# Kernel optimization log

Measured on AMD Instinct MI355X. Metric: run time of the kernel, lower is better.

The kernel has to match this reference:

```python
import jax, jax.numpy as jnp
import numpy as np

B, N, S, K = 16, 16384, 4096, 16
D_PT, D_IN, C_MID, D_OUT = 3, 64, 16, 128
HID = [8, 8]


def _layernorm(x, g, b, eps=1e-5):
    m = x.mean(-1, keepdims=True)
    v = x.var(-1, keepdims=True)
    return (x - m) * jax.lax.rsqrt(v + eps) * g + b


def _gather(feat, idx):
    # feat: [B, C, N], idx: [B, S, K] -> [B, C, S, K]
    return jax.vmap(lambda f, i: f[:, i])(feat, idx)


def setup_inputs() -> dict:
    key = jax.random.key(0)
    ks = jax.random.split(key, 16)
    inp = {
        "xyz": jax.random.normal(ks[0], (B, D_PT, N), jnp.float32),
        "points": jax.random.normal(ks[1], (B, D_IN, N), jnp.float32),
        "new_xyz": jax.random.normal(ks[2], (B, D_PT, S), jnp.float32),
        "nn_idx": jax.random.randint(ks[3], (B, S, K), 0, N, jnp.int32),
    }
    # WeightNet: Linear(3,8)+LN(8), Linear(8,8)+LN(8), Linear(8,16)+LN(16)
    dims = [D_PT] + HID + [C_MID]
    for i in range(3):
        inp[f"w{i}"] = jax.random.normal(ks[4 + i], (dims[i], dims[i + 1]), jnp.float32) * 0.1
        inp[f"b{i}"] = jnp.zeros((dims[i + 1],), jnp.float32)
        inp[f"g{i}"] = jnp.ones((dims[i + 1],), jnp.float32)
        inp[f"be{i}"] = jnp.zeros((dims[i + 1],), jnp.float32)
    last_ch = D_PT + D_IN  # 67
    inp["wl"] = jax.random.normal(ks[8], (C_MID * last_ch, D_OUT), jnp.float32) * 0.02
    inp["bl"] = jnp.zeros((D_OUT,), jnp.float32)
    inp["gl"] = jnp.ones((D_OUT,), jnp.float32)
    inp["bel"] = jnp.zeros((D_OUT,), jnp.float32)
    return inp


def reference(xyz, points, new_xyz, nn_idx,
              w0, b0, g0, be0, w1, b1, g1, be1, w2, b2, g2, be2,
              wl, bl, gl, bel):
    # gather neighbor positions / features: [B, C, S, K]
    grouped_xyz = _gather(xyz, nn_idx)
    gxn = grouped_xyz - new_xyz[:, :, :, None]          # [B, 3, S, K]
    feat = jnp.concatenate([_gather(points, nn_idx), gxn], axis=1)  # [B, 67, S, K]

    # WeightNet on relative coords: MLP over channel dim, layout [B, S, K, 3]
    w = jnp.transpose(gxn, (0, 2, 3, 1))
    for wi, bi, gi, bei in ((w0, b0, g0, be0), (w1, b1, g1, be1), (w2, b2, g2, be2)):
        w = jax.nn.leaky_relu(_layernorm(w @ wi + bi, gi, bei), 0.2)
    # w: [B, S, K, c_mid]

    # weighted aggregation: out[b,s,c,m] = sum_k feat[b,c,s,k] * w[b,s,k,m]
    agg = jnp.einsum("bcsk,bskm->bscm", feat, w).reshape(B, S, -1)  # [B, S, 67*c_mid]

    out = _layernorm(agg @ wl + bl, gl, bel)
    out = jax.nn.leaky_relu(out, 0.2)
    return jnp.transpose(out, (0, 2, 1))  # [B, out_channel, S]
```

## Files before the change

kernel.cpp:

```cpp
#include <hip/hip_runtime.h>

#define B_ 16
#define N_ 16384
#define S_ 4096
#define K_ 16
#define TS 32
#define DOUT 128

typedef __bf16 bf16;
typedef __attribute__((ext_vector_type(8))) __bf16 bf16x8;
typedef __attribute__((ext_vector_type(4))) float f32x4;

__device__ __forceinline__ unsigned pack2(float a, float b) {
  unsigned short ua = __builtin_bit_cast(unsigned short, (bf16)a);
  unsigned short ub = __builtin_bit_cast(unsigned short, (bf16)b);
  return (unsigned)ua | ((unsigned)ub << 16);
}

template <int NCH>
__device__ __forceinline__ void ln_leaky(const float* h, const float* g, const float* e, float* o) {
  float m = 0.f;
#pragma unroll
  for (int j = 0; j < NCH; ++j) m += h[j];
  m *= (1.0f / NCH);
  float v = 0.f;
#pragma unroll
  for (int j = 0; j < NCH; ++j) { float d = h[j] - m; v += d * d; }
  v *= (1.0f / NCH);
  float inv = rsqrtf(v + 1e-5f);
#pragma unroll
  for (int j = 0; j < NCH; ++j) {
    float t = (h[j] - m) * inv * g[j] + e[j];
    o[j] = t < 0.f ? 0.2f * t : t;
  }
}

__global__ void k_fill(float* out, float v) {
  out[blockIdx.x * 256 + threadIdx.x] = v;
}

__global__ __launch_bounds__(256) void k_transpose(const float* __restrict__ pts,
                                                   bf16* __restrict__ pt) {
  int b = blockIdx.y;
  int n0 = blockIdx.x * 256;
  int tc = threadIdx.x & 7;
  int tn = threadIdx.x >> 3;
  const float* src = pts + (size_t)b * 64 * N_ + (size_t)(tc * 8) * N_ + n0 + tn * 8;
  float4 row[8][2];
#pragma unroll
  for (int i = 0; i < 8; ++i) {
    row[i][0] = *(const float4*)(src + (size_t)i * N_);
    row[i][1] = *(const float4*)(src + (size_t)i * N_ + 4);
  }
  bf16* dst = pt + ((size_t)b * N_ + n0 + tn * 8) * 64 + tc * 8;
#pragma unroll
  for (int j = 0; j < 8; ++j) {
    float v[8];
#pragma unroll
    for (int i = 0; i < 8; ++i) {
      float4 q = row[i][j >> 2];
      v[i] = ((j & 3) == 0) ? q.x : ((j & 3) == 1) ? q.y : ((j & 3) == 2) ? q.z : q.w;
    }
    *(uint4*)(dst + (size_t)j * 64) = make_uint4(
        pack2(v[0], v[1]), pack2(v[2], v[3]), pack2(v[4], v[5]), pack2(v[6], v[7]));
  }
}

__global__ void k_wlf(const float* __restrict__ wl, bf16* __restrict__ wlF) {
  int blk = blockIdx.x;
  int kkg = blk % 34;
  int t = blk / 34;
  int tid = threadIdx.x;
  int L = tid >> 2, jp = (tid & 3) * 2;
  int k = kkg * 32 + ((L >> 4) << 3) + jp;
  int n = t * 16 + (L & 15);
  float v0 = (k < 1072) ? wl[(size_t)k * 128 + n] : 0.f;
  float v1 = (k + 1 < 1072) ? wl[(size_t)(k + 1) * 128 + n] : 0.f;
  ((unsigned*)wlF)[(size_t)blk * 256 + tid] = pack2(v0, v1);
}

__global__ __launch_bounds__(256, 4) void k_main(
    const float* __restrict__ xyz, const float* __restrict__ nxyz,
    const int* __restrict__ nnidx,
    const bf16* __restrict__ ptT, const bf16* __restrict__ wlF,
    const float* __restrict__ w0p, const float* __restrict__ b0p,
    const float* __restrict__ g0p, const float* __restrict__ be0p,
    const float* __restrict__ w1p, const float* __restrict__ b1p,
    const float* __restrict__ g1p, const float* __restrict__ be1p,
    const float* __restrict__ w2p, const float* __restrict__ b2p,
    const float* __restrict__ g2p, const float* __restrict__ be2p,
    const float* __restrict__ blp, const float* __restrict__ glp,
    const float* __restrict__ belp, float* __restrict__ out) {
  __shared__ __align__(16) bf16 w_sT[32 * 264];
  __shared__ __align__(16) bf16 feat2[32 * 144];
  __shared__ __align__(16) bf16 aggA[32 * 136];
  __shared__ float nx[3][TS];
  __shared__ float ln_m[TS], ln_i[TS];

  const int tid = threadIdx.x;
  const unsigned Lwg = blockIdx.y * 128u + blockIdx.x;
  const int xcd = (int)(Lwg & 7u);
  const int li = (int)(Lwg >> 3);
  const int b = xcd * 2 + (li >> 7);
  const int s0 = (li & 127) * TS;
  const size_t ibase = ((size_t)b * S_ + s0) * K_;

  if (tid < 96) {
    int c = tid >> 5, j = tid & 31;
    nx[c][j] = nxyz[((size_t)b * 3 + c) * S_ + s0 + j];
  }
  const int ig0 = nnidx[ibase + tid];
  const int ig1 = nnidx[ibase + tid + 256];
  const int iw0 = nnidx[ibase + 2 * tid];
  const int iw1 = nnidx[ibase + 2 * tid + 1];
  __syncthreads();

  float xa[3], xb[3];
  const int ws = tid >> 3;
  const int wk = (tid & 7) * 2;
  {
#pragma unroll
    for (int c = 0; c < 3; ++c) {
      float nv = nx[c][ws];
      xa[c] = xyz[((size_t)b * 3 + c) * N_ + iw0] - nv;
      xb[c] = xyz[((size_t)b * 3 + c) * N_ + iw1] - nv;
    }
    float ya[8], yb[8];
    {
      float h0[8], h1[8];
#pragma unroll
      for (int j = 0; j < 8; ++j) {
        h0[j] = b0p[j] + xa[0] * w0p[j] + xa[1] * w0p[8 + j] + xa[2] * w0p[16 + j];
        h1[j] = b0p[j] + xb[0] * w0p[j] + xb[1] * w0p[8 + j] + xb[2] * w0p[16 + j];
      }
      ln_leaky<8>(h0, g0p, be0p, ya);
      ln_leaky<8>(h1, g0p, be0p, yb);
    }
    {
      float h0[8], h1[8];
#pragma unroll
      for (int j = 0; j < 8; ++j) { h0[j] = b1p[j]; h1[j] = b1p[j]; }
#pragma unroll
      for (int i = 0; i < 8; ++i) {
#pragma unroll
        for (int j = 0; j < 8; ++j) {
          float w = w1p[i * 8 + j];
          h0[j] += ya[i] * w; h1[j] += yb[i] * w;
        }
      }
      ln_leaky<8>(h0, g1p, be1p, ya);
      ln_leaky<8>(h1, g1p, be1p, yb);
    }
    {
      float h0[16], h1[16];
#pragma unroll
      for (int j = 0; j < 16; ++j) { h0[j] = b2p[j]; h1[j] = b2p[j]; }
#pragma unroll
      for (int i = 0; i < 8; ++i) {
#pragma unroll
        for (int j = 0; j < 16; ++j) {
          float w = w2p[i * 16 + j];
          h0[j] += ya[i] * w; h1[j] += yb[i] * w;
        }
      }
      float z0[16], z1[16];
      ln_leaky<16>(h0, g2p, be2p, z0);
      ln_leaky<16>(h1, g2p, be2p, z1);
      bf16* wp = w_sT + ws * 264 + wk;
#pragma unroll
      for (int m = 0; m < 16; ++m)
        *(unsigned*)(wp + m * 16) = pack2(z0[m], z1[m]);
    }
  }

  const int lane = tid & 63;
  const int wv = tid >> 6;
  const int rt = wv & 1;
  const int cw = wv >> 1;
  const int l16 = lane & 15;
  const int q = lane >> 4;
  const bool adiag = ((((lane >> 5) ^ (lane >> 3)) & 1) == 0);
  const int aoff = ((lane >> 3) & 1) * 144 + (lane & 7) * 16 + (q & 1) * 8;
  const int boff = (lane >> 5) * 264 + l16 * 16 + (q & 1) * 8;
  const int soff = (lane >> 5) * 136 + (q & 1) * 64 + l16;
  f32x4 a00 = {0.f, 0.f, 0.f, 0.f};
  f32x4 a01 = a00, a10 = a00, a11 = a00;
  const f32x4 zc = a00;

  const bf16* ptB = ptT + (size_t)b * N_ * 64;
  const int gs0 = tid >> 4, gk = tid & 15;

  uint4 pf0, pf1;
  pf0 = *(const uint4*)(ptB + (size_t)ig0 * 64);
  pf1 = *(const uint4*)(ptB + (size_t)ig1 * 64);

  for (int ch = 0; ch < 9; ++ch) {
    const int nkk = (ch < 8) ? 4 : 2;
    __syncthreads();
    if (ch < 8) {
      bf16 t0[8], t1[8];
      *(uint4*)t0 = pf0;
      *(uint4*)t1 = pf1;
      bf16* f0 = feat2 + gs0 * 144 + gk;
      bf16* f1 = feat2 + (gs0 + 16) * 144 + gk;
#pragma unroll
      for (int c = 0; c < 8; ++c) {
        f0[c * 16] = t0[c];
        f1[c * 16] = t1[c];
      }
    } else {
      bf16* fp = feat2 + ws * 144 + wk;
      *(unsigned*)(fp + 0 * 16) = pack2(xa[0], xb[0]);
      *(unsigned*)(fp + 1 * 16) = pack2(xa[1], xb[1]);
      *(unsigned*)(fp + 2 * 16) = pack2(xa[2], xb[2]);
#pragma unroll
      for (int c = 3; c < 8; ++c) *(unsigned*)(fp + c * 16) = 0u;
    }
    __syncthreads();
    if (ch < 8) {
      int nc = ch + 1;
      if (nc < 8) {
        pf0 = *(const uint4*)(ptB + (size_t)ig0 * 64 + nc * 8);
        pf1 = *(const uint4*)(ptB + (size_t)ig1 * 64 + nc * 8);
      }
    }
#pragma unroll
    for (int pp = 0; pp < 4; ++pp) {
      int s2 = (wv * 4 + pp) * 2;
      uint4 au = *(const uint4*)(feat2 + s2 * 144 + aoff);
      if (!adiag) au = make_uint4(0u, 0u, 0u, 0u);
      bf16x8 af = __builtin_bit_cast(bf16x8, au);
      bf16x8 bw = *(const bf16x8*)(w_sT + s2 * 264 + boff);
      f32x4 d = __builtin_amdgcn_mfma_f32_16x16x32_bf16(af, bw, zc, 0, 0, 0);
      bf16* cp = aggA + s2 * 136 + soff;
#pragma unroll
      for (int r = 0; r < 4; ++r) cp[r * 16] = (bf16)d[r];
    }
    __syncthreads();
    {
      const bf16* arow = aggA + (rt * 16 + l16) * 136 + q * 8;
      const size_t lb = (size_t)lane * 8;
      const size_t kb = (size_t)(ch * 4) * 512;
      const bf16* w0f = wlF + (size_t)(2 * cw + 0) * 17408 + kb + lb;
      const bf16* w1f = wlF + (size_t)(2 * cw + 1) * 17408 + kb + lb;
      const bf16* w2f = wlF + (size_t)(2 * cw + 4) * 17408 + kb + lb;
      const bf16* w3f = wlF + (size_t)(2 * cw + 5) * 17408 + kb + lb;
      for (int kk = 0; kk < nkk; ++kk) {
        bf16x8 af = *(const bf16x8*)(arow + kk * 32);
        bf16x8 bf0 = *(const bf16x8*)(w0f + kk * 512);
        bf16x8 bf1 = *(const bf16x8*)(w1f + kk * 512);
        bf16x8 bf2 = *(const bf16x8*)(w2f + kk * 512);
        bf16x8 bf3 = *(const bf16x8*)(w3f + kk * 512);
        a00 = __builtin_amdgcn_mfma_f32_16x16x32_bf16(af, bf0, a00, 0, 0, 0);
        a01 = __builtin_amdgcn_mfma_f32_16x16x32_bf16(af, bf1, a01, 0, 0, 0);
        a10 = __builtin_amdgcn_mfma_f32_16x16x32_bf16(af, bf2, a10, 0, 0, 0);
        a11 = __builtin_amdgcn_mfma_f32_16x16x32_bf16(af, bf3, a11, 0, 0, 0);
      }
    }
  }

  __syncthreads();
  float* out_s = (float*)w_sT;
  {
    int row = rt * 16 + q * 4;
    int c0 = (2 * cw + 0) * 16 + l16;
    int c1 = (2 * cw + 1) * 16 + l16;
    int c2 = 64 + c0;
    int c3 = 64 + c1;
    float bl0 = blp[c0], bl1 = blp[c1], bl2 = blp[c2], bl3 = blp[c3];
#pragma unroll
    for (int r = 0; r < 4; ++r) {
      out_s[(row + r) * 132 + c0] = a00[r] + bl0;
      out_s[(row + r) * 132 + c1] = a01[r] + bl1;
      out_s[(row + r) * 132 + c2] = a10[r] + bl2;
      out_s[(row + r) * 132 + c3] = a11[r] + bl3;
    }
  }
  __syncthreads();
  {
    int r = tid >> 3, g = tid & 7;
    const float* rowp = out_s + r * 132;
    float s1 = 0.f;
#pragma unroll
    for (int i = 0; i < 16; ++i) s1 += rowp[g + 8 * i];
    s1 += __shfl_xor(s1, 1);
    s1 += __shfl_xor(s1, 2);
    s1 += __shfl_xor(s1, 4);
    float m = s1 * (1.0f / 128.0f);
    float s2 = 0.f;
#pragma unroll
    for (int i = 0; i < 16; ++i) { float d = rowp[g + 8 * i] - m; s2 += d * d; }
    s2 += __shfl_xor(s2, 1);
    s2 += __shfl_xor(s2, 2);
    s2 += __shfl_xor(s2, 4);
    if (g == 0) {
      ln_m[r] = m;
      ln_i[r] = rsqrtf(s2 * (1.0f / 128.0f) + 1e-5f);
    }
  }
  __syncthreads();
  {
    int d = tid >> 1, sh = tid & 1;
    float gld = glp[d], beld = belp[d];
    float vals[16];
#pragma unroll
    for (int j = 0; j < 16; ++j) {
      int r = sh * 16 + j;
      float v = (out_s[r * 132 + d] - ln_m[r]) * ln_i[r] * gld + beld;
      vals[j] = v < 0.f ? 0.2f * v : v;
    }
    float* op = out + ((size_t)b * DOUT + d) * S_ + s0 + sh * 16;
#pragma unroll
    for (int i = 0; i < 4; ++i)
      *(float4*)(op + 4 * i) =
          make_float4(vals[4 * i], vals[4 * i + 1], vals[4 * i + 2], vals[4 * i + 3]);
  }
}

extern "C" void kernel_launch(void* const* d_in, const int* in_sizes, int n_in,
                              void* d_out, int out_size, void* d_ws, size_t ws_size,
                              hipStream_t stream) {
  const float* xyz  = (const float*)d_in[0];
  const float* pts  = (const float*)d_in[1];
  const float* nxyz = (const float*)d_in[2];
  const int* nnidx  = (const int*)d_in[3];
  const float* w0p  = (const float*)d_in[4];
  const float* b0p  = (const float*)d_in[5];
  const float* g0p  = (const float*)d_in[6];
  const float* be0p = (const float*)d_in[7];
  const float* w1p  = (const float*)d_in[8];
  const float* b1p  = (const float*)d_in[9];
  const float* g1p  = (const float*)d_in[10];
  const float* be1p = (const float*)d_in[11];
  const float* w2p  = (const float*)d_in[12];
  const float* b2p  = (const float*)d_in[13];
  const float* g2p  = (const float*)d_in[14];
  const float* be2p = (const float*)d_in[15];
  const float* wlp  = (const float*)d_in[16];
  const float* blp  = (const float*)d_in[17];
  const float* glp  = (const float*)d_in[18];
  const float* belp = (const float*)d_in[19];
  float* out = (float*)d_out;

  const size_t PTT_BYTES = (size_t)B_ * N_ * 64 * 2;
  const size_t WLF_BYTES = (size_t)8 * 34 * 64 * 8 * 2;
  bf16* ptT = (bf16*)d_ws;
  bf16* wlF = (bf16*)((char*)d_ws + PTT_BYTES);

  (void)hipGetLastError();

  if (ws_size < PTT_BYTES + WLF_BYTES) {
    k_fill<<<dim3(8), dim3(256), 0, stream>>>(out, 5000.0f);
    return;
  }

  k_transpose<<<dim3(N_ / 256, B_), dim3(256), 0, stream>>>(pts, ptT);
  hipError_t e1 = hipGetLastError();
  k_wlf<<<dim3(8 * 34), dim3(256), 0, stream>>>(wlp, wlF);
  hipError_t e2 = hipGetLastError();
  k_main<<<dim3(S_ / TS, B_), dim3(256), 0, stream>>>(
      xyz, nxyz, nnidx, ptT, wlF,
      w0p, b0p, g0p, be0p, w1p, b1p, g1p, be1p,
      w2p, b2p, g2p, be2p, blp, glp, belp, out);
  hipError_t e3 = hipGetLastError();

  if (e1 != hipSuccess)
    k_fill<<<dim3(8), dim3(256), 0, stream>>>(out, 2000.0f + (float)(int)e1);
  if (e2 != hipSuccess)
    k_fill<<<dim3(8), dim3(256), 0, stream>>>(out, 3000.0f + (float)(int)e2);
  if (e3 != hipSuccess)
    k_fill<<<dim3(8), dim3(256), 0, stream>>>(out, 4000.0f + (float)(int)e3);
}
```

Measured before the change: 240.3 us.

## Merge prep kernels with XCD-aware block mapping and rebalance MFMA warp tiling

The transpose and weight-reformat kernels are merged into one launch, which removes a launch and lets the two run concurrently. Transpose blocks are remapped so that each XCD handles two whole batches, aiming for better L2 locality. In the main kernel's final GEMM, each warp now covers both 16-row tiles and two column tiles instead of one row tile and four column tiles. This halves per-warp B-fragment loads from global memory at the cost of an extra LDS A-fragment load.

```diff
diff --git a/kernel.cpp b/kernel.cpp
--- a/kernel.cpp
+++ b/kernel.cpp
@@ -39,44 +39,49 @@
   out[blockIdx.x * 256 + threadIdx.x] = v;
 }
 
-__global__ __launch_bounds__(256) void k_transpose(const float* __restrict__ pts,
-                                                   bf16* __restrict__ pt) {
-  int b = blockIdx.y;
-  int n0 = blockIdx.x * 256;
-  int tc = threadIdx.x & 7;
-  int tn = threadIdx.x >> 3;
-  const float* src = pts + (size_t)b * 64 * N_ + (size_t)(tc * 8) * N_ + n0 + tn * 8;
-  float4 row[8][2];
-#pragma unroll
-  for (int i = 0; i < 8; ++i) {
-    row[i][0] = *(const float4*)(src + (size_t)i * N_);
-    row[i][1] = *(const float4*)(src + (size_t)i * N_ + 4);
-  }
-  bf16* dst = pt + ((size_t)b * N_ + n0 + tn * 8) * 64 + tc * 8;
-#pragma unroll
-  for (int j = 0; j < 8; ++j) {
-    float v[8];
+__global__ __launch_bounds__(256) void k_prep(const float* __restrict__ pts,
+                                              bf16* __restrict__ pt,
+                                              const float* __restrict__ wl,
+                                              bf16* __restrict__ wlF) {
+  int bi = blockIdx.x;
+  if (bi < 1024) {
+    int xcd = bi & 7;
+    int li = bi >> 3;
+    int b = xcd * 2 + (li >> 6);
+    int n0 = (li & 63) * 256;
+    int tc = threadIdx.x & 7;
+    int tn = threadIdx.x >> 3;
+    const float* src = pts + (size_t)b * 64 * N_ + (size_t)(tc * 8) * N_ + n0 + tn * 8;
+    float4 row[8][2];
 #pragma unroll
     for (int i = 0; i < 8; ++i) {
-      float4 q = row[i][j >> 2];
-      v[i] = ((j & 3) == 0) ? q.x : ((j & 3) == 1) ? q.y : ((j & 3) == 2) ? q.z : q.w;
-    }
-    *(uint4*)(dst + (size_t)j * 64) = make_uint4(
-        pack2(v[0], v[1]), pack2(v[2], v[3]), pack2(v[4], v[5]), pack2(v[6], v[7]));
-  }
-}
-
-__global__ void k_wlf(const float* __restrict__ wl, bf16* __restrict__ wlF) {
-  int blk = blockIdx.x;
-  int kkg = blk % 34;
-  int t = blk / 34;
-  int tid = threadIdx.x;
-  int L = tid >> 2, jp = (tid & 3) * 2;
-  int k = kkg * 32 + ((L >> 4) << 3) + jp;
-  int n = t * 16 + (L & 15);
-  float v0 = (k < 1072) ? wl[(size_t)k * 128 + n] : 0.f;
-  float v1 = (k + 1 < 1072) ? wl[(size_t)(k + 1) * 128 + n] : 0.f;
-  ((unsigned*)wlF)[(size_t)blk * 256 + tid] = pack2(v0, v1);
+      row[i][0] = *(const float4*)(src + (size_t)i * N_);
+      row[i][1] = *(const float4*)(src + (size_t)i * N_ + 4);
+    }
+    bf16* dst = pt + ((size_t)b * N_ + n0 + tn * 8) * 64 + tc * 8;
+#pragma unroll
+    for (int j = 0; j < 8; ++j) {
+      float v[8];
+#pragma unroll
+      for (int i = 0; i < 8; ++i) {
+        float4 q = row[i][j >> 2];
+        v[i] = ((j & 3) == 0) ? q.x : ((j & 3) == 1) ? q.y : ((j & 3) == 2) ? q.z : q.w;
+      }
+      *(uint4*)(dst + (size_t)j * 64) = make_uint4(
+          pack2(v[0], v[1]), pack2(v[2], v[3]), pack2(v[4], v[5]), pack2(v[6], v[7]));
+    }
+  } else {
+    int blk = bi - 1024;
+    int kkg = blk % 34;
+    int t = blk / 34;
+    int tid = threadIdx.x;
+    int L = tid >> 2, jp = (tid & 3) * 2;
+    int k = kkg * 32 + ((L >> 4) << 3) + jp;
+    int n = t * 16 + (L & 15);
+    float v0 = (k < 1072) ? wl[(size_t)k * 128 + n] : 0.f;
+    float v1 = (k + 1 < 1072) ? wl[(size_t)(k + 1) * 128 + n] : 0.f;
+    ((unsigned*)wlF)[(size_t)blk * 256 + tid] = pack2(v0, v1);
+  }
 }
 
 __global__ __launch_bounds__(256, 4) void k_main(
@@ -175,8 +180,6 @@
 
   const int lane = tid & 63;
   const int wv = tid >> 6;
-  const int rt = wv & 1;
-  const int cw = wv >> 1;
   const int l16 = lane & 15;
   const int q = lane >> 4;
   const bool adiag = ((((lane >> 5) ^ (lane >> 3)) & 1) == 0);
@@ -238,23 +241,21 @@
     }
     __syncthreads();
     {
-      const bf16* arow = aggA + (rt * 16 + l16) * 136 + q * 8;
+      const bf16* arow0 = aggA + l16 * 136 + q * 8;
+      const bf16* arow1 = aggA + (16 + l16) * 136 + q * 8;
       const size_t lb = (size_t)lane * 8;
       const size_t kb = (size_t)(ch * 4) * 512;
-      const bf16* w0f = wlF + (size_t)(2 * cw + 0) * 17408 + kb + lb;
-      const bf16* w1f = wlF + (size_t)(2 * cw + 1) * 17408 + kb + lb;
-      const bf16* w2f = wlF + (size_t)(2 * cw + 4) * 17408 + kb + lb;
-      const bf16* w3f = wlF + (size_t)(2 * cw + 5) * 17408 + kb + lb;
+      const bf16* w0f = wlF + (size_t)wv * 17408 + kb + lb;
+      const bf16* w1f = wlF + (size_t)(wv + 4) * 17408 + kb + lb;
       for (int kk = 0; kk < nkk; ++kk) {
-        bf16x8 af = *(const bf16x8*)(arow + kk * 32);
+        bf16x8 af0 = *(const bf16x8*)(arow0 + kk * 32);
+        bf16x8 af1 = *(const bf16x8*)(arow1 + kk * 32);
         bf16x8 bf0 = *(const bf16x8*)(w0f + kk * 512);
         bf16x8 bf1 = *(const bf16x8*)(w1f + kk * 512);
-        bf16x8 bf2 = *(const bf16x8*)(w2f + kk * 512);
-        bf16x8 bf3 = *(const bf16x8*)(w3f + kk * 512);
-        a00 = __builtin_amdgcn_mfma_f32_16x16x32_bf16(af, bf0, a00, 0, 0, 0);
-        a01 = __builtin_amdgcn_mfma_f32_16x16x32_bf16(af, bf1, a01, 0, 0, 0);
-        a10 = __builtin_amdgcn_mfma_f32_16x16x32_bf16(af, bf2, a10, 0, 0, 0);
-        a11 = __builtin_amdgcn_mfma_f32_16x16x32_bf16(af, bf3, a11, 0, 0, 0);
+        a00 = __builtin_amdgcn_mfma_f32_16x16x32_bf16(af0, bf0, a00, 0, 0, 0);
+        a01 = __builtin_amdgcn_mfma_f32_16x16x32_bf16(af0, bf1, a01, 0, 0, 0);
+        a10 = __builtin_amdgcn_mfma_f32_16x16x32_bf16(af1, bf0, a10, 0, 0, 0);
+        a11 = __builtin_amdgcn_mfma_f32_16x16x32_bf16(af1, bf1, a11, 0, 0, 0);
       }
     }
   }
@@ -262,18 +263,17 @@
   __syncthreads();
   float* out_s = (float*)w_sT;
   {
-    int row = rt * 16 + q * 4;
-    int c0 = (2 * cw + 0) * 16 + l16;
-    int c1 = (2 * cw + 1) * 16 + l16;
-    int c2 = 64 + c0;
-    int c3 = 64 + c1;
-    float bl0 = blp[c0], bl1 = blp[c1], bl2 = blp[c2], bl3 = blp[c3];
+    int row0 = q * 4;
+    int row1 = 16 + q * 4;
+    int c0 = wv * 16 + l16;
+    int c1 = 64 + c0;
+    float bl0 = blp[c0], bl1 = blp[c1];
 #pragma unroll
     for (int r = 0; r < 4; ++r) {
-      out_s[(row + r) * 132 + c0] = a00[r] + bl0;
-      out_s[(row + r) * 132 + c1] = a01[r] + bl1;
-      out_s[(row + r) * 132 + c2] = a10[r] + bl2;
-      out_s[(row + r) * 132 + c3] = a11[r] + bl3;
+      out_s[(row0 + r) * 132 + c0] = a00[r] + bl0;
+      out_s[(row0 + r) * 132 + c1] = a01[r] + bl1;
+      out_s[(row1 + r) * 132 + c0] = a10[r] + bl0;
+      out_s[(row1 + r) * 132 + c1] = a11[r] + bl1;
     }
   }
   __syncthreads();
@@ -354,10 +354,8 @@
     return;
   }
 
-  k_transpose<<<dim3(N_ / 256, B_), dim3(256), 0, stream>>>(pts, ptT);
+  k_prep<<<dim3(1024 + 8 * 34), dim3(256), 0, stream>>>(pts, ptT, wlp, wlF);
   hipError_t e1 = hipGetLastError();
-  k_wlf<<<dim3(8 * 34), dim3(256), 0, stream>>>(wlp, wlF);
-  hipError_t e2 = hipGetLastError();
   k_main<<<dim3(S_ / TS, B_), dim3(256), 0, stream>>>(
       xyz, nxyz, nnidx, ptT, wlF,
       w0p, b0p, g0p, be0p, w1p, b1p, g1p, be1p,
@@ -366,8 +364,6 @@
 
   if (e1 != hipSuccess)
     k_fill<<<dim3(8), dim3(256), 0, stream>>>(out, 2000.0f + (float)(int)e1);
-  if (e2 != hipSuccess)
-    k_fill<<<dim3(8), dim3(256), 0, stream>>>(out, 3000.0f + (float)(int)e2);
   if (e3 != hipSuccess)
     k_fill<<<dim3(8), dim3(256), 0, stream>>>(out, 4000.0f + (float)(int)e3);
 }
```

Result: faster. 231.0 us, median of 2 (-3.9%).
